# Kernel optimization log

Measured on AMD Instinct MI355X. Metric: run time of the kernel, lower is better.

Reference implementation:

```python
import jax, jax.numpy as jnp
import numpy as np
from jax import lax

# STE sign: forward maps x>=0 -> +1, x<0 -> -1 (matches XORQuantizeSTE)
@jax.custom_vjp
def ste_sign(x):
    return jnp.where(x >= 0, jnp.ones_like(x), -jnp.ones_like(x))

def _ste_fwd(x):
    return ste_sign(x), None

def _ste_bwd(_, g):
    return (g,)  # identity pass-through

ste_sign.defvjp(_ste_fwd, _ste_bwd)


def _xor_quant(x, w):
    """Per-layer XNOR-Net quantization: alpha = mean|W| scales both
    binarized activation and binarized weight (as in the wrapper's hook
    + binarization())."""
    alpha = jnp.mean(jnp.abs(w))
    return alpha * ste_sign(x), alpha * ste_sign(w)


def _conv(x, w, b, stride):
    y = lax.conv_general_dilated(
        x, w, window_strides=(stride, stride), padding=((1, 1), (1, 1)),
        dimension_numbers=('NCHW', 'OIHW', 'NCHW'))
    return y + b[None, :, None, None]


def setup_inputs() -> dict:
    key = jax.random.key(0)
    ks = jax.random.split(key, 9)
    f32 = jnp.float32
    x = jax.random.normal(ks[0], (32, 3, 224, 224), dtype=f32)
    w1 = jax.random.normal(ks[1], (64, 3, 3, 3), dtype=f32) * 0.1
    b1 = jax.random.normal(ks[2], (64,), dtype=f32) * 0.01
    w2 = jax.random.normal(ks[3], (128, 64, 3, 3), dtype=f32) * 0.05
    b2 = jax.random.normal(ks[4], (128,), dtype=f32) * 0.01
    w3 = jax.random.normal(ks[5], (256, 128, 3, 3), dtype=f32) * 0.03
    b3 = jax.random.normal(ks[6], (256,), dtype=f32) * 0.01
    wf = jax.random.normal(ks[7], (1000, 256), dtype=f32) * 0.05
    bf = jax.random.normal(ks[8], (1000,), dtype=f32) * 0.01
    return {'x': x, 'w1': w1, 'b1': b1, 'w2': w2, 'b2': b2,
            'w3': w3, 'b3': b3, 'wf': wf, 'bf': bf}


def reference(x, w1, b1, w2, b2, w3, b3, wf, bf):
    # layer 1: binarize activation + weight with shared alpha, dense conv
    xq, wq = _xor_quant(x, w1)
    h = jnp.clip(_conv(xq, wq, b1, 2), -1.0, 1.0)   # [32,64,112,112]
    xq, wq = _xor_quant(h, w2)
    h = jnp.clip(_conv(xq, wq, b2, 2), -1.0, 1.0)   # [32,128,56,56]
    xq, wq = _xor_quant(h, w3)
    h = jnp.clip(_conv(xq, wq, b3, 2), -1.0, 1.0)   # [32,256,28,28]
    h = jnp.mean(h, axis=(2, 3))                     # global avg pool [32,256]
    xq, wq = _xor_quant(h, wf)
    return xq @ wq.T + bf                            # [32,1000]
```

## Files before the change

### kernel.cpp

```cpp
#include <hip/hip_runtime.h>
#include <stdint.h>
#include <math.h>


#define WP2_OFF    2048ull
#define WP3T_OFF   16384ull
#define WFP_OFF    65536ull
#define PART_OFF   100352ull
#define P1_OFF     102400ull
#define P2_OFF     3313664ull
#define POOLP_OFF  4919296ull

__global__ __launch_bounds__(256) void k1_conv1_pack(
    const float* __restrict__ x,  const float* __restrict__ w1, const float* __restrict__ b1,
    const float* __restrict__ w2, const float* __restrict__ w3, const float* __restrict__ wf,
    uint64_t* __restrict__ wp2, uint64_t* __restrict__ wp3t, uint64_t* __restrict__ wfp,
    double* __restrict__ part, uint64_t* __restrict__ p1)
{
    const int tid = threadIdx.x, lane = tid & 63, wid = tid >> 6, bid = blockIdx.x;
    if (bid >= 160) {
        __shared__ float4   xf4[1512];
        __shared__ uint32_t xb[216];
        __shared__ uint32_t xms[448];
        __shared__ uint32_t wm[64];
        __shared__ double   a2s;
        const float* xf = (const float*)xf4;

        int cb = bid - 160;
        int n = cb / 28, hb = cb % 28;
        int ho0 = hb * 4;
        int hi0 = 2 * ho0 - 1;

        if (wid == 0) {
            double s = 0.0;
            #pragma unroll
            for (int i = 0; i < 27; i++) s += fabs((double)w1[lane + i*64]);
            #pragma unroll
            for (int off = 1; off < 64; off <<= 1) s += __shfl_xor(s, off, 64);
            if (lane == 0) { double a = s / 1728.0; a2s = a * a; }
        } else if (wid == 1) {
            uint32_t m = 0;
            for (int t = 0; t < 27; t++) {
                int ci = t / 9, r = t % 9, kh = r / 3, kw = r % 3;
                if (w1[((lane*3 + ci)*3 + kh)*3 + kw] >= 0.f) m |= (1u << t);
            }
            wm[lane] = m;
        }
        const float4* xg = (const float4*)x;
        for (int i = tid; i < 1512; i += 256) {
            int seg = i / 56, f4 = i % 56;
            int ci = seg / 9, r = seg % 9;
            int hi = hi0 + r;
            float4 v = make_float4(0.f, 0.f, 0.f, 0.f);
            if ((unsigned)hi < 224u) v = xg[((n*3 + ci)*224 + hi)*56 + f4];
            xf4[i] = v;
        }
        __syncthreads();

        uint32_t wmr = wm[lane];
        int Mn, Ml;
        {
            double a2 = a2s, b = (double)b1[lane];
            int k = (int)ceil(-b / a2);
            k = max(-27, min(28, k));
            while (k > -27 && (a2 * (double)(k - 1) + b >= 0.0)) k--;
            while (k <= 27 && !(a2 * (double)k + b >= 0.0)) k++;
            int cntT  = __popc(wmr & 0x1C0E07u);
            int cntL  = __popc(wmr & 0x1249249u);
            int cntTL = __popc(wmr & 0x40201u);
            bool topw = (hb == 0 && wid == 0);
            if (topw) {
                Mn = ((18 - k) >> 1) + 9 - cntT;
                Ml = ((12 - k) >> 1) + cntL + 6 - cntT + cntTL;
            } else {
                Mn = (27 - k) >> 1;
                Ml = ((18 - k) >> 1) + cntL;
            }
        }

        if (tid < 189) {
            int seg = tid / 7, j = tid % 7;
            uint32_t u = 0;
            #pragma unroll
            for (int k = 0; k < 32; k++) {
                int o = (k + tid) & 31;
                if (xf[seg*224 + j*32 + o] >= 0.f) u |= (1u << o);
            }
            xb[seg*8 + j] = u;
        } else if (tid < 216) {
            xb[(tid - 189)*8 + 7] = 0u;
        }
        __syncthreads();

        for (int pass = 0; pass < 2; pass++) {
            int s = tid + pass*256;
            if (s >= 448) break;
            int dho = s / 112, wo = s % 112;
            int c0 = 2*wo - 1;
            uint32_t xm = 0;
            if (wo > 0) {
                int w0 = c0 >> 5, sh = c0 & 31;
                #pragma unroll
                for (int ci = 0; ci < 3; ci++)
                    #pragma unroll
                    for (int kh = 0; kh < 3; kh++) {
                        int seg = ci*9 + 2*dho + kh;
                        uint64_t dw = (uint64_t)xb[seg*8 + w0]
                                    | ((uint64_t)xb[seg*8 + w0 + 1] << 32);
                        xm |= (uint32_t)((dw >> sh) & 7u) << (ci*9 + kh*3);
                    }
            } else {
                #pragma unroll
                for (int ci = 0; ci < 3; ci++)
                    #pragma unroll
                    for (int kh = 0; kh < 3; kh++) {
                        int seg = ci*9 + 2*dho + kh;
                        xm |= ((xb[seg*8] << 1) & 6u) << (ci*9 + kh*3);
                    }
            }
            xms[s] = xm;
        }
        __syncthreads();

        {
            int hop = ho0 + wid;
            const uint32_t* xrow = &xms[wid*112];
            uint64_t r0 = 0, r1 = 0;
            {
                int mm = __popc(xrow[0] ^ wmr);
                uint64_t bal = __ballot(mm <= Ml);
                r0 = (lane == 0) ? bal : r0;
            }
            for (int wo = 1; wo < 64; wo++) {
                int mm = __popc(xrow[wo] ^ wmr);
                uint64_t bal = __ballot(mm <= Mn);
                r0 = (lane == wo) ? bal : r0;
            }
            for (int wo = 64; wo < 112; wo++) {
                int mm = __popc(xrow[wo] ^ wmr);
                uint64_t bal = __ballot(mm <= Mn);
                r1 = (lane == (wo - 64)) ? bal : r1;
            }
            uint64_t* __restrict__ prow = p1 + ((size_t)(n*112 + hop))*112;
            prow[lane] = r0;
            if (lane < 48) prow[64 + lane] = r1;
        }
    } else {
        int rel = bid;
        if (rel < 96) {
            __shared__ double sd[256];
            int t = rel >> 5, c = rel & 31;
            const float* w; int n;
            if (t == 0)      { w = w2; n = 128*64*9; }
            else if (t == 1) { w = w3; n = 256*128*9; }
            else             { w = wf; n = 1000*256; }
            int per = (n + 31) / 32;
            int lo = c * per, hi = min(n, lo + per);
            double s0 = 0.0, s1 = 0.0, s2 = 0.0, s3 = 0.0;
            int i = lo + tid;
            for (; i + 768 < hi; i += 1024) {
                s0 += fabs((double)w[i]);
                s1 += fabs((double)w[i + 256]);
                s2 += fabs((double)w[i + 512]);
                s3 += fabs((double)w[i + 768]);
            }
            for (; i < hi; i += 256) s0 += fabs((double)w[i]);
            sd[tid] = (s0 + s1) + (s2 + s3);
            __syncthreads();
            for (int off = 128; off > 0; off >>= 1) {
                if (tid < off) sd[tid] += sd[tid + off];
                __syncthreads();
            }
            if (tid == 0) part[(t + 1)*32 + c] = sd[0];
        }
        int gw = rel * 4 + wid;
        const int nw = 640;
        for (int w = gw; w < 1152; w += nw) {
            int co = w / 9, tap = w % 9, kh = tap / 3, kw = tap % 3;
            uint64_t b = __ballot(w2[((co*64 + lane)*3 + kh)*3 + kw] >= 0.f);
            if (lane == 0) wp2[w] = b;
        }
        for (int w = gw; w < 4608; w += nw) {
            int co = w / 18, r = w % 18, tap = r / 2, half = r & 1;
            int kh = tap / 3, kw = tap % 3;
            uint64_t b = __ballot(w3[((co*128 + half*64 + lane)*3 + kh)*3 + kw] >= 0.f);
            if (lane == 0) wp3t[(tap*2 + half)*256 + co] = b;
        }
        for (int w = gw; w < 4000; w += nw) {
            int o = w >> 2, j = w & 3;
            uint64_t b = __ballot(wf[o*256 + j*64 + lane] >= 0.f);
            if (lane == 0) wfp[w] = b;
        }
    }
}

__global__ __launch_bounds__(256) void k2_conv2(
    const uint64_t* __restrict__ p1, const float* __restrict__ b2,
    const double* __restrict__ part, const uint64_t* __restrict__ wp2g,
    uint32_t* __restrict__ p2)
{
    __shared__ uint64_t wp[1152];
    __shared__ uint64_t xs[1152];
    __shared__ int      M[128*4];
    const int tid = threadIdx.x, lane = tid & 63;

    for (int i = tid; i < 1152; i += 256) wp[i] = wp2g[i];
    for (int i = tid; i < 1152; i += 256) {
        int t = i >> 7, pl = i & 127;
        int pos = blockIdx.x * 128 + pl;
        int wo = pos % 56, t1 = pos / 56;
        int ho = t1 % 56, n = t1 / 56;
        int kh = t / 3, kw = t % 3;
        int hi = 2*ho + kh - 1, wi = 2*wo + kw - 1;
        bool ok = ((unsigned)hi < 112u) && ((unsigned)wi < 112u);
        xs[i] = ok ? p1[(n*112 + hi)*112 + wi] : 0ull;
    }
    __syncthreads();
    if (tid < 128) {
        int co = tid;
        double s = 0.0;
        for (int j = 0; j < 32; j++) s += part[32 + j];
        double a = s / (double)(128*64*9);
        double a2 = a * a, b = (double)b2[co];
        int k = (int)ceil(-b / a2);
        k = max(-577, min(578, k));
        while (k > -577 && (a2 * (double)(k - 1) + b >= 0.0)) k--;
        while (k <= 577 && !(a2 * (double)k + b >= 0.0)) k++;
        uint32_t P[9];
        #pragma unroll
        for (int t = 0; t < 9; t++) P[t] = __popcll(wp[co*9 + t]);
        int cT = P[0] + P[1] + P[2];
        int cL = P[0] + P[3] + P[6];
        int cC = P[0];
        #pragma unroll
        for (int cfg = 0; cfg < 4; cfg++) {
            int isT = cfg & 1, isL = (cfg >> 1) & 1;
            int V = 9 - 3*isT - 3*isL + (isT & isL);
            int corr = isT*cT + isL*cL - (isT & isL)*cC;
            int dtab = 64*V + 2*corr;
            M[co*4 + cfg] = (dtab - k) >> 1;
        }
    }
    __syncthreads();

    int q = tid >> 6;
    int co0 = q * 32;
    int pos0 = blockIdx.x * 128 + lane;
    int pos1 = pos0 + 64;
    int wo0 = pos0 % 56, ho0 = (pos0 / 56) % 56;
    int wo1 = pos1 % 56, ho1 = (pos1 / 56) % 56;
    int cfg0 = (ho0 == 0 ? 1 : 0) | (wo0 == 0 ? 2 : 0);
    int cfg1 = (ho1 == 0 ? 1 : 0) | (wo1 == 0 ? 2 : 0);
    uint64_t xv0[9], xv1[9];
    #pragma unroll
    for (int t = 0; t < 9; t++) { xv0[t] = xs[t*128 + lane]; xv1[t] = xs[t*128 + 64 + lane]; }
    uint32_t bits0 = 0, bits1 = 0;
    for (int c = 0; c < 32; c++) {
        int co = co0 + c;
        int mm0 = 0, mm1 = 0;
        #pragma unroll
        for (int t = 0; t < 9; t++) {
            uint64_t w = wp[co*9 + t];
            mm0 += __popcll(xv0[t] ^ w);
            mm1 += __popcll(xv1[t] ^ w);
        }
        if (mm0 <= M[co*4 + cfg0]) bits0 |= (1u << c);
        if (mm1 <= M[co*4 + cfg1]) bits1 |= (1u << c);
    }
    p2[pos0*4 + q] = bits0;
    p2[pos1*4 + q] = bits1;
}

__global__ __launch_bounds__(256) void k3_conv3pool(
    const uint64_t* __restrict__ p2, const float* __restrict__ b3,
    const double* __restrict__ part, const uint64_t* __restrict__ wp3t,
    double* __restrict__ partial)
{
    __shared__ uint64_t xs[28*18];
    const int tid = threadIdx.x;
    int n = blockIdx.x / 28, ho = blockIdx.x % 28;

    double s = 0.0;
    for (int j = 0; j < 32; j++) s += part[64 + j];
    double a = s / (double)(256*128*9);
    double a2 = a * a;

    uint64_t w[18];
    #pragma unroll
    for (int i = 0; i < 18; i++) w[i] = wp3t[i*256 + tid];
    uint32_t P[9];
    #pragma unroll
    for (int t = 0; t < 9; t++) P[t] = __popcll(w[2*t]) + __popcll(w[2*t+1]);

    for (int i = tid; i < 504; i += 256) {
        int wo = i / 18, r = i % 18;
        int tap = r / 2, half = r % 2;
        int kh = tap / 3, kw = tap % 3;
        int hi = 2*ho + kh - 1, wi = 2*wo + kw - 1;
        bool ok = ((unsigned)hi < 56u) && ((unsigned)wi < 56u);
        xs[i] = ok ? p2[(size_t)((n*56 + hi)*56 + wi)*2 + half] : 0ull;
    }
    __syncthreads();

    bool htop = (ho == 0);
    int rv = htop ? 2 : 3;
    double bc = (double)b3[tid];
    double sum = 0.0;
    for (int wo = 0; wo < 28; wo++) {
        int mm = 0;
        #pragma unroll
        for (int t = 0; t < 18; t++)
            mm += __popcll(xs[wo*18 + t] ^ w[t]);
        bool wl = (wo == 0);
        int cv = wl ? 2 : 3;
        int corr = 0;
        if (htop) corr += P[0] + P[1] + P[2];
        if (wl)   corr += P[0] + P[3] + P[6];
        if (htop && wl) corr -= P[0];
        int dot = 128*(rv*cv) - 2*mm + 2*corr;
        double h = a2 * (double)dot + bc;
        h = fmin(fmax(h, -1.0), 1.0);
        sum += h;
    }
    partial[(size_t)(n*28 + ho)*256 + tid] = sum;
}

__global__ __launch_bounds__(256) void k4_poolfc(
    const double* __restrict__ partial, const uint64_t* __restrict__ wfp,
    const float* __restrict__ bf, const double* __restrict__ part,
    float* __restrict__ out)
{
    __shared__ uint64_t spl[4];
    const int tid = threadIdx.x, lane = tid & 63;
    int n = blockIdx.x;
    double s = 0.0;
    for (int c = 0; c < 28; c++) s += partial[(size_t)(n*28 + c)*256 + tid];
    uint64_t bal = __ballot((s / 784.0) >= 0.0);
    if (lane == 0) spl[tid >> 6] = bal;

    double sa = 0.0;
    for (int j = 0; j < 32; j++) sa += part[96 + j];
    double a = sa / (double)(1000*256);
    double aa = a * a;
    __syncthreads();
    uint64_t s0 = spl[0], s1 = spl[1], s2 = spl[2], s3 = spl[3];
    for (int o = tid; o < 1000; o += 256) {
        int m = __popcll(s0 ^ wfp[o*4]) + __popcll(s1 ^ wfp[o*4+1])
              + __popcll(s2 ^ wfp[o*4+2]) + __popcll(s3 ^ wfp[o*4+3]);
        out[n*1000 + o] = (float)(aa * (double)(256 - 2*m) + (double)bf[o]);
    }
}

extern "C" void kernel_launch(void* const* d_in, const int* in_sizes, int n_in,
                              void* d_out, int out_size, void* d_ws, size_t ws_size,
                              hipStream_t stream) {
    const float* x  = (const float*)d_in[0];
    const float* w1 = (const float*)d_in[1];
    const float* b1 = (const float*)d_in[2];
    const float* w2 = (const float*)d_in[3];
    const float* b2 = (const float*)d_in[4];
    const float* w3 = (const float*)d_in[5];
    const float* b3 = (const float*)d_in[6];
    const float* wf = (const float*)d_in[7];
    const float* bf = (const float*)d_in[8];

    char* ws = (char*)d_ws;
    uint64_t* wp2    = (uint64_t*)(ws + WP2_OFF);
    uint64_t* wp3t   = (uint64_t*)(ws + WP3T_OFF);
    uint64_t* wfp    = (uint64_t*)(ws + WFP_OFF);
    double*   part   = (double*)  (ws + PART_OFF);
    uint64_t* p1     = (uint64_t*)(ws + P1_OFF);
    uint32_t* p2     = (uint32_t*)(ws + P2_OFF);
    double*   poolp  = (double*)  (ws + POOLP_OFF);
    float*    out    = (float*)   d_out;

    hipLaunchKernelGGL(k1_conv1_pack, dim3(1056), dim3(256), 0, stream,
                       x, w1, b1, w2, w3, wf, wp2, wp3t, wfp, part, p1);
    hipLaunchKernelGGL(k2_conv2,      dim3(784),  dim3(256), 0, stream,
                       p1, b2, part, wp2, p2);
    hipLaunchKernelGGL(k3_conv3pool,  dim3(896),  dim3(256), 0, stream,
                       (const uint64_t*)p2, b3, part, wp3t, poolp);
    hipLaunchKernelGGL(k4_poolfc,     dim3(32),   dim3(256), 0, stream,
                       poolp, wfp, bf, part, out);
}
```

Baseline: 144.5 us.

## Fuse pool+FC into conv3 via last-block atomic counter; skip clamp when safe

Removes the separate pool/FC kernel launch. A per-image atomic counter, reset in conv2, lets the last of the 28 conv3 blocks for each image reduce the partials and compute the binarized FC output. Conv3 also gets a fast path that sums the popcounts algebraically when bias plus or minus the maximum dot magnitude cannot hit the clamp. That path drops the per-position double math and clamp, at the cost of a runtime branch and threadfence/atomic overhead.

Measured after the change: 212.2 us. 46.8% more time.

```diff
diff --git a/kernel.cpp b/kernel.cpp
--- a/kernel.cpp
+++ b/kernel.cpp
@@ -7,6 +7,7 @@
 #define WP3T_OFF   16384ull
 #define WFP_OFF    65536ull
 #define PART_OFF   100352ull
+#define CNT_OFF    101376ull
 #define P1_OFF     102400ull
 #define P2_OFF     3313664ull
 #define POOLP_OFF  4919296ull
@@ -197,12 +198,14 @@
 __global__ __launch_bounds__(256) void k2_conv2(
     const uint64_t* __restrict__ p1, const float* __restrict__ b2,
     const double* __restrict__ part, const uint64_t* __restrict__ wp2g,
-    uint32_t* __restrict__ p2)
+    uint32_t* __restrict__ p2, uint32_t* __restrict__ cnt)
 {
     __shared__ uint64_t wp[1152];
     __shared__ uint64_t xs[1152];
     __shared__ int      M[128*4];
     const int tid = threadIdx.x, lane = tid & 63;
+
+    if (blockIdx.x == 0 && tid < 32) cnt[tid] = 0;
 
     for (int i = tid; i < 1152; i += 256) wp[i] = wp2g[i];
     for (int i = tid; i < 1152; i += 256) {
@@ -271,12 +274,16 @@
     p2[pos1*4 + q] = bits1;
 }
 
-__global__ __launch_bounds__(256) void k3_conv3pool(
+__global__ __launch_bounds__(256) void k3_conv3poolfc(
     const uint64_t* __restrict__ p2, const float* __restrict__ b3,
     const double* __restrict__ part, const uint64_t* __restrict__ wp3t,
-    double* __restrict__ partial)
+    double* __restrict__ partial, uint32_t* __restrict__ cnt,
+    const uint64_t* __restrict__ wfp, const float* __restrict__ bf,
+    float* __restrict__ out)
 {
     __shared__ uint64_t xs[28*18];
+    __shared__ uint64_t spl[4];
+    __shared__ int lastf;
     const int tid = threadIdx.x;
     int n = blockIdx.x / 28, ho = blockIdx.x % 28;
 
@@ -305,48 +312,71 @@
     bool htop = (ho == 0);
     int rv = htop ? 2 : 3;
     double bc = (double)b3[tid];
-    double sum = 0.0;
-    for (int wo = 0; wo < 28; wo++) {
-        int mm = 0;
-        #pragma unroll
-        for (int t = 0; t < 18; t++)
-            mm += __popcll(xs[wo*18 + t] ^ w[t]);
-        bool wl = (wo == 0);
-        int cv = wl ? 2 : 3;
-        int corr = 0;
-        if (htop) corr += P[0] + P[1] + P[2];
-        if (wl)   corr += P[0] + P[3] + P[6];
-        if (htop && wl) corr -= P[0];
-        int dot = 128*(rv*cv) - 2*mm + 2*corr;
-        double h = a2 * (double)dot + bc;
-        h = fmin(fmax(h, -1.0), 1.0);
-        sum += h;
+    int cT = P[0] + P[1] + P[2];
+    int cL = P[0] + P[3] + P[6];
+    double sum;
+    bool fastok = (a2 * 1152.0 + bc <= 1.0) && (bc - a2 * 1152.0 >= -1.0);
+    if (fastok) {
+        int mm0 = 0, mmacc = 0;
+        for (int wo = 0; wo < 28; wo++) {
+            int mm = 0;
+            #pragma unroll
+            for (int t = 0; t < 18; t++)
+                mm += __popcll(xs[wo*18 + t] ^ w[t]);
+            if (wo == 0) mm0 = mm; else mmacc += mm;
+        }
+        int corr_n = htop ? cT : 0;
+        int corr_l = corr_n + cL - (htop ? P[0] : 0);
+        int dotsum = 27*(128*rv*3 + 2*corr_n)
+                   + (128*rv*2 + 2*corr_l)
+                   - 2*(mmacc + mm0);
+        sum = a2 * (double)dotsum + 28.0 * bc;
+    } else {
+        sum = 0.0;
+        for (int wo = 0; wo < 28; wo++) {
+            int mm = 0;
+            #pragma unroll
+            for (int t = 0; t < 18; t++)
+                mm += __popcll(xs[wo*18 + t] ^ w[t]);
+            bool wl = (wo == 0);
+            int cv = wl ? 2 : 3;
+            int corr = 0;
+            if (htop) corr += cT;
+            if (wl)   corr += cL;
+            if (htop && wl) corr -= P[0];
+            int dot = 128*(rv*cv) - 2*mm + 2*corr;
+            double h = a2 * (double)dot + bc;
+            h = fmin(fmax(h, -1.0), 1.0);
+            sum += h;
+        }
     }
     partial[(size_t)(n*28 + ho)*256 + tid] = sum;
-}
-
-__global__ __launch_bounds__(256) void k4_poolfc(
-    const double* __restrict__ partial, const uint64_t* __restrict__ wfp,
-    const float* __restrict__ bf, const double* __restrict__ part,
-    float* __restrict__ out)
-{
-    __shared__ uint64_t spl[4];
-    const int tid = threadIdx.x, lane = tid & 63;
-    int n = blockIdx.x;
-    double s = 0.0;
-    for (int c = 0; c < 28; c++) s += partial[(size_t)(n*28 + c)*256 + tid];
-    uint64_t bal = __ballot((s / 784.0) >= 0.0);
+
+    __threadfence();
+    __syncthreads();
+    if (tid == 0) {
+        int old = atomicAdd(&cnt[n], 1u);
+        lastf = (old == 27) ? 1 : 0;
+    }
+    __syncthreads();
+    if (!lastf) return;
+    __threadfence();
+
+    const int lane = tid & 63;
+    double ps = 0.0;
+    for (int c = 0; c < 28; c++) ps += partial[(size_t)(n*28 + c)*256 + tid];
+    uint64_t bal = __ballot((ps / 784.0) >= 0.0);
     if (lane == 0) spl[tid >> 6] = bal;
 
     double sa = 0.0;
     for (int j = 0; j < 32; j++) sa += part[96 + j];
-    double a = sa / (double)(1000*256);
-    double aa = a * a;
-    __syncthreads();
-    uint64_t s0 = spl[0], s1 = spl[1], s2 = spl[2], s3 = spl[3];
+    double af = sa / (double)(1000*256);
+    double aa = af * af;
+    __syncthreads();
+    uint64_t t0 = spl[0], t1 = spl[1], t2 = spl[2], t3 = spl[3];
     for (int o = tid; o < 1000; o += 256) {
-        int m = __popcll(s0 ^ wfp[o*4]) + __popcll(s1 ^ wfp[o*4+1])
-              + __popcll(s2 ^ wfp[o*4+2]) + __popcll(s3 ^ wfp[o*4+3]);
+        int m = __popcll(t0 ^ wfp[o*4]) + __popcll(t1 ^ wfp[o*4+1])
+              + __popcll(t2 ^ wfp[o*4+2]) + __popcll(t3 ^ wfp[o*4+3]);
         out[n*1000 + o] = (float)(aa * (double)(256 - 2*m) + (double)bf[o]);
     }
 }
@@ -369,6 +399,7 @@
     uint64_t* wp3t   = (uint64_t*)(ws + WP3T_OFF);
     uint64_t* wfp    = (uint64_t*)(ws + WFP_OFF);
     double*   part   = (double*)  (ws + PART_OFF);
+    uint32_t* cnt    = (uint32_t*)(ws + CNT_OFF);
     uint64_t* p1     = (uint64_t*)(ws + P1_OFF);
     uint32_t* p2     = (uint32_t*)(ws + P2_OFF);
     double*   poolp  = (double*)  (ws + POOLP_OFF);
@@ -377,9 +408,8 @@
     hipLaunchKernelGGL(k1_conv1_pack, dim3(1056), dim3(256), 0, stream,
                        x, w1, b1, w2, w3, wf, wp2, wp3t, wfp, part, p1);
     hipLaunchKernelGGL(k2_conv2,      dim3(784),  dim3(256), 0, stream,
-                       p1, b2, part, wp2, p2);
-    hipLaunchKernelGGL(k3_conv3pool,  dim3(896),  dim3(256), 0, stream,
-                       (const uint64_t*)p2, b3, part, wp3t, poolp);
-    hipLaunchKernelGGL(k4_poolfc,     dim3(32),   dim3(256), 0, stream,
-                       poolp, wfp, bf, part, out);
+                       p1, b2, part, wp2, p2, cnt);
+    hipLaunchKernelGGL(k3_conv3poolfc, dim3(896), dim3(256), 0, stream,
+                       (const uint64_t*)p2, b3, part, wp3t, poolp, cnt,
+                       wfp, bf, out);
 }
```
